# Optimization experiments

Hardware: AMD Instinct MI355X
Metric: run time of the kernel (lower is better)

The kernel has to match this reference:

```python
import jax, jax.numpy as jnp
import numpy as np

B, N = 32, 1000
HID, COM = 256, 64
T_LEN, NOP = 288, 3
NVAL, TP_D, CS_D, TIME_D = 9, 2, 4, 4
IN_C = CS_D + TP_D + NVAL            # 15, competition GAT input
IN_CO = IN_C + COM                    # 79, cooperation GAT input
OBS = TIME_D + TP_D + CS_D + 2 * COM + NVAL  # 147
K_D = K_F = 500                       # int(0.5*N + 0.5)
TEMP = 1.0
NEG = jnp.float32(-1e8)


def setup_inputs() -> dict:
    key = jax.random.key(0)
    ks = jax.random.split(key, 24)
    def nrm(k, shp, scale=0.05):
        return (jax.random.normal(k, shp, dtype=jnp.float32) * scale)
    return {
        "time_idx": jax.random.randint(ks[0], (B, N), 0, T_LEN, dtype=jnp.int32),
        "op_idx": jax.random.randint(ks[1], (B, N), 0, NOP, dtype=jnp.int32),
        "value_feats": jax.random.normal(ks[2], (B, N, NVAL), dtype=jnp.float32),
        "dpcs_mark": jax.random.randint(ks[3], (B, N, 1), 0, 2) > 0,
        "adj_comp": jax.random.randint(ks[4], (B, N, N), 0, 2) > 0,
        "adj_coop": jax.random.randint(ks[5], (B, N, N), 0, 2) > 0,
        "distance": jax.random.uniform(ks[6], (N, N), dtype=jnp.float32),
        "time_tab": jax.random.uniform(ks[7], (T_LEN, TIME_D), dtype=jnp.float32),
        "tp_tab": jax.random.uniform(ks[8], (NOP, TP_D), dtype=jnp.float32),
        "cs_tab": jax.random.uniform(ks[9], (N, CS_D), dtype=jnp.float32),
        "Wc": nrm(ks[10], (IN_C, COM)),
        "asrc_c": nrm(ks[11], (COM,)),
        "adst_c": nrm(ks[12], (COM,)),
        "wd_c": jnp.float32(0.1),
        "Wco": nrm(ks[13], (IN_CO, COM)),
        "asrc_co": nrm(ks[14], (COM,)),
        "adst_co": nrm(ks[15], (COM,)),
        "wd_co": jnp.float32(0.1),
        "Wp": nrm(ks[16], (OBS, HID)),
        "bp": jnp.zeros((HID,), dtype=jnp.float32),
        "vpd": nrm(ks[17], (HID,)),
        "vpf": nrm(ks[18], (HID,)),
    }


def gat(x, W, a_src, a_dst, w_d, adj, dist):
    """Single-head GAT over dense boolean adjacency. adj[b,j,i] True => edge j->i."""
    h = jnp.einsum("bnf,fd->bnd", x, W)                       # (B,N,D)
    e = (jnp.einsum("bid,d->bi", h, a_dst)[:, :, None]        # dst term
         + jnp.einsum("bjd,d->bj", h, a_src)[:, None, :]      # src term
         + w_d * dist.T[None])                                 # dist[j,i] edge feat
    e = jax.nn.leaky_relu(e, 0.2)
    mask = jnp.swapaxes(adj, 1, 2)                             # (B, dst i, src j)
    e = jnp.where(mask, e, NEG)
    alpha = jax.nn.softmax(e, axis=-1)
    alpha = jnp.where(mask, alpha, 0.0)                        # isolated nodes -> 0
    return jax.nn.elu(jnp.einsum("bij,bjd->bid", alpha, h))


def gated_pool(x_p, scores, valid, k, temp):
    scores = scores - scores.max(axis=1, keepdims=True)
    scores = jnp.where(valid, scores, NEG)                     # (B,N,1)
    val_topk = jax.lax.top_k(scores[..., 0], k)[0]             # (B,k)
    min_topk = val_topk.min(axis=-1)[:, None, None]
    scores = jnp.where(scores < min_topk, NEG, scores)
    w = jax.nn.softmax(scores / temp, axis=1)
    xg = x_p * w
    return jnp.concatenate([xg.sum(axis=1), xg.max(axis=1)], axis=-1)  # (B,2H)


def reference(time_idx, op_idx, value_feats, dpcs_mark, adj_comp, adj_coop,
              distance, time_tab, tp_tab, cs_tab, Wc, asrc_c, adst_c, wd_c,
              Wco, asrc_co, adst_co, wd_co, Wp, bp, vpd, vpf):
    time_e = time_tab[time_idx]                                # (B,N,4)
    tp_e = tp_tab[op_idx]                                      # (B,N,2)
    cs_e = jnp.broadcast_to(cs_tab[None], (B, N, CS_D))        # (B,N,4)
    vf_det = jax.lax.stop_gradient(value_feats)
    x = jnp.concatenate([cs_e, tp_e, vf_det], axis=-1)         # (B,N,15)
    comp_reps = gat(x, Wc, asrc_c, adst_c, wd_c, adj_comp, distance)
    x_m = jnp.concatenate([x, comp_reps], axis=-1)             # (B,N,79)
    coop_reps = gat(x_m, Wco, asrc_co, adst_co, wd_co, adj_coop, distance)
    sag = jnp.concatenate([time_e, cs_e, tp_e, value_feats, comp_reps, coop_reps], axis=-1)
    x_p = jnp.einsum("bnf,fh->bnh", sag, Wp) + bp              # (B,N,HID)
    scores_d = jnp.einsum("bnh,h->bn", x_p, vpd)[..., None]
    s_d = gated_pool(x_p, scores_d, dpcs_mark, K_D, TEMP)
    scores_f = jnp.einsum("bnh,h->bn", x_p, vpf)[..., None]
    s_f = gated_pool(x_p, scores_f, ~dpcs_mark, K_F, TEMP)
    return jnp.concatenate([s_f, s_d], axis=-1)                # (B, 4*HID)
```

## Files before the change

### kernel.cpp

```cpp
#include <hip/hip_runtime.h>
#include <hip/hip_bf16.h>

#define NB 32
#define NN 1000
#define COMD 64
#define HIDD 256
#define KSEL 500
#define TI 16
#define GATX ((NN + TI - 1) / TI)
#define PACKX 32
#define NSPL 32
#define ROWS 32
#define DSTRIDE 1024

#define PB_AQ1  0
#define PB_DT   1024
#define PB_WP   1280
#define PB_WCO  1320
#define PB_MISC 1344
#define PB_EMB  1345
#define PB_N    (PB_EMB + NB * NN / 4)

typedef __hip_bfloat16 bf16;
typedef unsigned long long u64;
typedef __attribute__((ext_vector_type(4))) float f32x4;
typedef __attribute__((ext_vector_type(8))) short s16x8;
typedef __attribute__((ext_vector_type(4))) short s16x4;
typedef __attribute__((ext_vector_type(4))) unsigned short u16x4;
typedef __attribute__((ext_vector_type(2))) unsigned long long u64x2;

__device__ __forceinline__ float b2f(bf16 x){ return __bfloat162float(x); }

template<bool F32>
__device__ __forceinline__ float ldf(const void* p, long i){
  return F32 ? ((const float*)p)[i] : b2f(((const bf16*)p)[i]);
}
__device__ __forceinline__ float ldr(const void* p, long i, int f32){
  return f32 ? ((const float*)p)[i] : b2f(((const bf16*)p)[i]);
}
template<bool BINT>
__device__ __forceinline__ bool ldb(const void* p, long i){
  return BINT ? (((const int*)p)[i] != 0) : (((const unsigned char*)p)[i] != 0);
}

__device__ __forceinline__ float wave_sum(float v){
#pragma unroll
  for (int o = 32; o > 0; o >>= 1) v += __shfl_down(v, o, 64);
  return v;
}
__device__ __forceinline__ float wave_bsum(float v){
#pragma unroll
  for (int o = 32; o > 0; o >>= 1) v += __shfl_xor(v, o, 64);
  return v;
}
__device__ __forceinline__ float wave_bmax(float v){
#pragma unroll
  for (int o = 32; o > 0; o >>= 1) v = fmaxf(v, __shfl_xor(v, o, 64));
  return v;
}
__device__ __forceinline__ int wave_bsum_i(int v){
#pragma unroll
  for (int o = 32; o > 0; o >>= 1) v += __shfl_xor(v, o, 64);
  return v;
}
__device__ __forceinline__ unsigned fkey(float f){
  unsigned u = __float_as_uint(f);
  return (u & 0x80000000u) ? ~u : (u | 0x80000000u);
}
__device__ __forceinline__ void split_bf(float v, short& hi, short& lo){
  unsigned u = __float_as_uint(v);
  float hf = __uint_as_float(u & 0xFFFF0000u);
  hi = (short)(u >> 16);
  float r = v - hf;
  lo = (short)(__float_as_uint(r) >> 16);
}
__device__ __forceinline__ short f2bs(float v){
  bf16 h = __float2bfloat16(v);
  short s; __builtin_memcpy(&s, &h, 2); return s;
}
__device__ __forceinline__ void hB_write(short* hB_hi, short* hB_lo,
                                         int b, int n, int ch, float v){
  int kb = n >> 5, g4 = (n >> 3) & 3, u = n & 7;
  long off = ((((long)b * 32 + kb) * 4 + g4) * 64 + ch) * 8 + u;
  short hi, lo; split_bf(v, hi, lo);
  hB_hi[off] = hi; hB_lo[off] = lo;
}
__device__ __forceinline__ void sniff2(const void* dist, const void* adjc,
                                       int lane, int& f32, int& as_int){
  unsigned wdist = ((const unsigned*)dist)[lane];
  unsigned wadj  = ((const unsigned*)adjc)[lane];
  f32 = (__ballot((wdist & 0xFFFFu) >= 0x8000u) != 0ull) ? 1 : 0;
  as_int = (__ballot(wadj > 1u) == 0ull) ? 1 : 0;
}

#define SMEM_BYTES 8704

template<bool F32>
__device__ __forceinline__ void dist_t_role(const void* dist, bf16* distTb,
                                            int rel, void* sm){
  bf16 (*tile)[68] = (bf16 (*)[68])sm;
  int t = threadIdx.x;
  int wv = t >> 6, lane = t & 63;
  int it = (rel & 15) * 64, jt = (rel >> 4) * 64;
#pragma unroll
  for (int r = 0; r < 16; ++r){
    int jl = r * 4 + wv;
    int j = jt + jl, i = it + lane;
    float v = (j < NN && i < NN) ? ldf<F32>(dist, (long)j * NN + i) : 0.f;
    tile[jl][lane] = __float2bfloat16(v);
  }
  __syncthreads();
#pragma unroll
  for (int r = 0; r < 16; ++r){
    int il = r * 4 + wv;
    int i = it + il, j = jt + lane;
    if (i < NN) distTb[(long)i * DSTRIDE + j] = tile[lane][il];
  }
}
template<bool BINT>
__device__ __forceinline__ void adjq_role(const void* adj, u64* adjQ,
                                          int rel, void* sm){
  u64 (*aw)[33] = (u64 (*)[33])sm;
  int t = threadIdx.x;
  int wv = t >> 6, lane = t & 63;
  int j0 = (rel & 31) * 32;
  int b  = rel >> 5;
  int ch3 = (192 + lane < 250) ? (192 + lane) : 249;
  int chk[4] = { lane, 64 + lane, 128 + lane, ch3 };
  long row0;
  {
    int j = j0 + wv * 8;
    int jc = (j < NN) ? j : (NN - 1);
    row0 = ((long)b * NN + jc) * (long)NN;
  }
  if (BINT){
    const int* base = (const int*)adj;
    uint4 cur[4], nxt[4];
#pragma unroll
    for (int c = 0; c < 4; ++c)
      cur[c] = *(const uint4*)(base + row0 + (long)chk[c] * 4);
#pragma unroll
    for (int r = 0; r < 8; ++r){
      if (r < 7){
        int j2 = j0 + wv * 8 + r + 1;
        int jc2 = (j2 < NN) ? j2 : (NN - 1);
        long row2 = ((long)b * NN + jc2) * (long)NN;
#pragma unroll
        for (int c = 0; c < 4; ++c)
          nxt[c] = *(const uint4*)(base + row2 + (long)chk[c] * 4);
      }
      int j = j0 + wv * 8 + r;
#pragma unroll
      for (int c = 0; c < 4; ++c){
        u64 bal0 = __ballot(cur[c].x != 0u);
        u64 bal1 = __ballot(cur[c].y != 0u);
        u64 bal2 = __ballot(cur[c].z != 0u);
        u64 bal3 = __ballot(cur[c].w != 0u);
        if (lane < 4){
          u64 w = 0;
          if (j < NN){
            int sh = 16 * lane;
            w = ((bal0 >> sh) & 0xFFFFull)
              | (((bal1 >> sh) & 0xFFFFull) << 16)
              | (((bal2 >> sh) & 0xFFFFull) << 32)
              | (((bal3 >> sh) & 0xFFFFull) << 48);
          }
          aw[c * 4 + lane][wv * 8 + r] = w;
        }
      }
      if (r < 7){
#pragma unroll
        for (int c = 0; c < 4; ++c) cur[c] = nxt[c];
      }
    }
  } else {
    const unsigned char* base = (const unsigned char*)adj;
    unsigned cur[4], nxt[4];
#pragma unroll
    for (int c = 0; c < 4; ++c)
      cur[c] = *(const unsigned*)(base + row0 + (long)chk[c] * 4);
#pragma unroll
    for (int r = 0; r < 8; ++r){
      if (r < 7){
        int j2 = j0 + wv * 8 + r + 1;
        int jc2 = (j2 < NN) ? j2 : (NN - 1);
        long row2 = ((long)b * NN + jc2) * (long)NN;
#pragma unroll
        for (int c = 0; c < 4; ++c)
          nxt[c] = *(const unsigned*)(base + row2 + (long)chk[c] * 4);
      }
      int j = j0 + wv * 8 + r;
#pragma unroll
      for (int c = 0; c < 4; ++c){
        u64 bal0 = __ballot((cur[c] & 0xFFu) != 0u);
        u64 bal1 = __ballot((cur[c] & 0xFF00u) != 0u);
        u64 bal2 = __ballot((cur[c] & 0xFF0000u) != 0u);
        u64 bal3 = __ballot((cur[c] & 0xFF000000u) != 0u);
        if (lane < 4){
          u64 w = 0;
          if (j < NN){
            int sh = 16 * lane;
            w = ((bal0 >> sh) & 0xFFFFull)
              | (((bal1 >> sh) & 0xFFFFull) << 16)
              | (((bal2 >> sh) & 0xFFFFull) << 32)
              | (((bal3 >> sh) & 0xFFFFull) << 48);
          }
          aw[c * 4 + lane][wv * 8 + r] = w;
        }
      }
      if (r < 7){
#pragma unroll
        for (int c = 0; c < 4; ++c) cur[c] = nxt[c];
      }
    }
  }
  __syncthreads();
#pragma unroll
  for (int rr = 0; rr < 2; ++rr){
    int w2 = t + rr * 256;
    int iw = w2 >> 5, jloc = w2 & 31;
    adjQ[((long)b * 16 + iw) * 1024 + j0 + jloc] = aw[iw][jloc];
  }
}
template<bool F32>
__device__ __forceinline__ void wp_role(const void* Wp, const void* vpd, const void* vpf,
                        short* WpB_hi, short* WpB_lo, float* wv_ws, int rel){
  int t = threadIdx.x;
  int g = t >> 6, lane = t & 63;
  int f = rel * 4 + g;
  float wrow[4];
#pragma unroll
  for (int r = 0; r < 4; ++r){
    int ch = r * 64 + lane;
    wrow[r] = (f < 147) ? ldf<F32>(Wp, (long)f * HIDD + ch) : 0.f;
  }
  int kb = f >> 5, q = (f >> 3) & 3, u = f & 7;
#pragma unroll
  for (int r = 0; r < 4; ++r){
    int ch = r * 64 + lane;
    long off = (((long)(kb * 4 + q)) * 256 + ch) * 8 + u;
    short hi, lo; split_bf(wrow[r], hi, lo);
    WpB_hi[off] = hi; WpB_lo[off] = lo;
  }
  float ad = 0.f, af = 0.f;
#pragma unroll
  for (int r = 0; r < 4; ++r){
    int ch = r * 64 + lane;
    ad += wrow[r] * ldf<F32>(vpd, ch);
    af += wrow[r] * ldf<F32>(vpf, ch);
  }
  ad = wave_bsum(ad); af = wave_bsum(af);
  if (lane == 0){ wv_ws[f] = ad; wv_ws[160 + f] = af; }
}
template<bool F32>
__device__ __forceinline__ void wco_role(const void* Wco, const void* asrc, const void* adst,
                         short* WcoB_hi, short* WcoB_lo, float* pvco, int rel){
  int t = threadIdx.x;
  int g = t >> 6, lane = t & 63;
  int f = rel * 4 + g;
  float w = (f < 79) ? ldf<F32>(Wco, (long)f * COMD + lane) : 0.f;
  int kb = f >> 5, q = (f >> 3) & 3, u = f & 7;
  long off = (((long)(kb * 4 + q)) * 64 + lane) * 8 + u;
  short hi, lo; split_bf(w, hi, lo);
  WcoB_hi[off] = hi; WcoB_lo[off] = lo;
  float dd = wave_bsum(w * ldf<F32>(adst, lane));
  float ss = wave_bsum(w * ldf<F32>(asrc, lane));
  if (lane == 0){ pvco[f] = dd; pvco[96 + f] = ss; }
}
template<bool F32>
__device__ __forceinline__ void misc_role(const void* wdc, const void* wdco,
                          const void* bp, const void* vpd, const void* vpf,
                          int f32, int as_int,
                          int* flags, float* wd_ws, float* wv_ws){
  int t = threadIdx.x;
  if (t >= 64) return;
  int lane = t;
  float ad = 0.f, af = 0.f;
#pragma unroll
  for (int r = 0; r < 4; ++r){
    int ch = r * 64 + lane;
    float bb = ldf<F32>(bp, ch);
    ad += bb * ldf<F32>(vpd, ch);
    af += bb * ldf<F32>(vpf, ch);
  }
  ad = wave_bsum(ad); af = wave_bsum(af);
  if (lane == 0){
    wv_ws[320] = ad; wv_ws[321] = af;
    wd_ws[0] = ldf<F32>(wdc, 0);
    wd_ws[1] = ldf<F32>(wdco, 0);
    flags[0] = f32; flags[1] = as_int;
  }
}
template<bool F32>
__device__ __forceinline__ void embed_body(
    const int* op_idx, const void* vf, const void* cs_tab, const void* tp_tab,
    const void* Wc, const void* asrc, const void* adst,
    float* x_out, short* hB_hi, short* hB_lo, float* ed_out, float* es_out,
    int rel){
  int t = threadIdx.x;
  int w = t >> 6, lane = t & 63;
  int g = rel * 4 + w;
  int b = g / NN, n = g - b * NN;
  int op = op_idx[g];
  float xv = 0.f, hacc = 0.f;
#pragma unroll
  for (int f = 0; f < 15; ++f){
    float x_f;
    if (f < 4)      x_f = ldf<F32>(cs_tab, n * 4 + f);
    else if (f < 6) x_f = ldf<F32>(tp_tab, op * 2 + (f - 4));
    else            x_f = ldf<F32>(vf, (long)g * 9 + (f - 6));
    if (lane == f) xv = x_f;
    hacc += x_f * ldf<F32>(Wc, f * COMD + lane);
  }
  if (lane < 15) x_out[g * 15 + lane] = xv;
  hB_write(hB_hi, hB_lo, b, n, lane, hacc);
  float sd = wave_sum(hacc * ldf<F32>(adst, lane));
  float ss = wave_sum(hacc * ldf<F32>(asrc, lane));
  if (lane == 0){ ed_out[g] = sd; es_out[g] = ss; }
}
__global__ void __launch_bounds__(256) k_prep(
    const void* dist, const void* adj_comp,
    const void* wdc, const void* wdco,
    const void* Wp, const void* vpd, const void* vpf, const void* bp,
    const void* Wco, const void* asrc_co, const void* adst_co,
    const int* op_idx, const void* vfeat, const void* cs_tab, const void* tp_tab,
    const void* Wc, const void* asrc_c, const void* adst_c,
    int* flags, float* wd_ws, bf16* distTb, u64* adjQc,
    short* WpB_hi, short* WpB_lo, float* wv_ws,
    short* WcoB_hi, short* WcoB_lo, float* pvco,
    float* x_ws, short* hB_hi, short* hB_lo, float* ed_c, float* es_c){
  __shared__ __attribute__((aligned(16))) char smem[SMEM_BYTES];
  int blk = blockIdx.x;
  int f32, as_int;
  sniff2(dist, adj_comp, threadIdx.x & 63, f32, as_int);
  if (blk < PB_DT){
    if (as_int) adjq_role<true >(adj_comp, adjQc, blk - PB_AQ1, smem);
    else        adjq_role<false>(adj_comp, adjQc, blk - PB_AQ1, smem);
  } else if (blk < PB_WP){
    if (f32) dist_t_role<true >(dist, distTb, blk - PB_DT, smem);
    else     dist_t_role<false>(dist, distTb, blk - PB_DT, smem);
  } else if (blk < PB_WCO){
    if (f32) wp_role<true >(Wp, vpd, vpf, WpB_hi, WpB_lo, wv_ws, blk - PB_WP);
    else     wp_role<false>(Wp, vpd, vpf, WpB_hi, WpB_lo, wv_ws, blk - PB_WP);
  } else if (blk < PB_MISC){
    if (f32) wco_role<true >(Wco, asrc_co, adst_co, WcoB_hi, WcoB_lo, pvco, blk - PB_WCO);
    else     wco_role<false>(Wco, asrc_co, adst_co, WcoB_hi, WcoB_lo, pvco, blk - PB_WCO);
  } else if (blk < PB_EMB){
    if (f32) misc_role<true >(wdc, wdco, bp, vpd, vpf, f32, as_int, flags, wd_ws, wv_ws);
    else     misc_role<false>(wdc, wdco, bp, vpd, vpf, f32, as_int, flags, wd_ws, wv_ws);
  } else {
    if (f32) embed_body<true >(op_idx, vfeat, cs_tab, tp_tab, Wc, asrc_c, adst_c,
                               x_ws, hB_hi, hB_lo, ed_c, es_c, blk - PB_EMB);
    else     embed_body<false>(op_idx, vfeat, cs_tab, tp_tab, Wc, asrc_c, adst_c,
                               x_ws, hB_hi, hB_lo, ed_c, es_c, blk - PB_EMB);
  }
}

template<int MODE>
__device__ __forceinline__ void gat_body(
    const float* __restrict__ ed, const float* __restrict__ es,
    const float* __restrict__ wd_ws, int wd_idx, const u64* __restrict__ adjQ,
    const bf16* __restrict__ distTb,
    const short* __restrict__ hB_hi, const short* __restrict__ hB_lo,
    float* __restrict__ reps,
    const int* __restrict__ flags, const void* adj_raw, u64* adjQ_out,
    const float* __restrict__ x_ws,
    const short* __restrict__ WcoB_hi, const short* __restrict__ WcoB_lo,
    const float* __restrict__ pvco,
    short* hB2_hi, short* hB2_lo, float* ed_o, float* es_o,
    const int* __restrict__ time_idx, const int* __restrict__ op_idx,
    const void* vf, const void* time_tab, const void* cs_tab, const void* tp_tab,
    const float* __restrict__ comp,
    const short* __restrict__ WpB_hi, const short* __restrict__ WpB_lo,
    const float* __restrict__ wv_ws, const void* bp,
    float* x_p, float* scf_o, float* scd_o){
  __shared__ short pA[32 * 544] __attribute__((aligned(16)));
  __shared__ float redz[TI][4];
  __shared__ float esred[4];
  if (MODE == 0 && blockIdx.x >= GATX){
    int rel = (blockIdx.x - GATX) * NB + blockIdx.y;
    if (flags[1]) adjq_role<true >(adj_raw, adjQ_out, rel, (void*)pA);
    else          adjq_role<false>(adj_raw, adjQ_out, rel, (void*)pA);
    return;
  }
  int t = threadIdx.x;
  int wv = t >> 6, lane = t & 63;
  int b = blockIdx.y;
  int i0 = blockIdx.x * TI;
  float wd = wd_ws[wd_idx];
  int iw = i0 >> 6;
  int sb2 = (i0 & 63) >> 2;
  int j0 = t * 4;

  const u64* aq = adjQ + ((long)b * 16 + iw) * 1024 + j0;
  u64x2 wA = *(const u64x2*)&aq[0];
  u64x2 wB = *(const u64x2*)&aq[2];
  u64 wsh[4] = { wA[0] >> sb2, wA[1] >> sb2, wB[0] >> sb2, wB[1] >> sb2 };
  float4 es4 = *(const float4*)&es[(long)b * NN + j0];
  float esv[4] = {es4.x, es4.y, es4.z, es4.w};
  float esm = -1e30f;
#pragma unroll
  for (int c = 0; c < 4; ++c)
    esm = fmaxf(esm, (j0 + c < NN) ? esv[c] : -1e30f);
  esm = wave_bmax(esm);
  if (lane == 0) esred[wv] = esm;

  float ed_i[TI]; float edm = -1e30f;
#pragma unroll
  for (int ti = 0; ti < TI; ++ti){
    int i = i0 + ti;
    float ev = ed[(long)b * NN + ((i < NN) ? i : (NN - 1))];
    ed_i[ti] = ev;
    edm = fmaxf(edm, (i < NN) ? ev : -1e30f);
  }
  __syncthreads();
  float M = fmaxf(fmaxf(esred[0], esred[1]), fmaxf(esred[2], esred[3]))
            + edm + fmaxf(wd, 0.f);
  M = fmaxf(M, 0.f);

  float p[TI][4];
  const bf16* dbase = distTb + j0;
#pragma unroll
  for (int ti = 0; ti < TI; ++ti){
    int i = i0 + ti;
    int ic = (i < NN) ? i : (NN - 1);
    u16x4 d4 = *(const u16x4*)&dbase[(long)ic * DSTRIDE];
    float edti = ed_i[ti];
    int psh = 16 * (ti & 3) + (ti >> 2);
#pragma unroll
    for (int c = 0; c < 4; ++c){
      float d = __uint_as_float((unsigned)d4[c] << 16);
      float v = edti + esv[c] + wd * d;
      v = fmaxf(v, 0.2f * v);
      bool edge = (wsh[c] >> psh) & 1ull;
      float e = edge ? v : -1e30f;
      p[ti][c] = __expf(e - M);
    }
  }

  int kbw = 8 * wv + (lane >> 3);
  int qw = (lane >> 1) & 3;
  int u0 = 4 * (lane & 1);
  int wbase = kbw * 544 + qw * 136 + u0;
#pragma unroll
  for (int ti = 0; ti < TI; ++ti){
    float zs = p[ti][0] + p[ti][1] + p[ti][2] + p[ti][3];
    zs = wave_bsum(zs);
    if (lane == 0) redz[ti][wv] = zs;
    s16x4 s4 = { f2bs(p[ti][0]), f2bs(p[ti][1]), f2bs(p[ti][2]), f2bs(p[ti][3]) };
    *(s16x4*)&pA[wbase + ti * 8] = s4;
  }
  __syncthreads();

  int q = lane >> 4, m = lane & 15;
  int abase = q * 136 + m * 8;
  int ch = wv * 16 + m;
  const short* bh = hB_hi + (long)b * 65536 + ((long)q * 64 + ch) * 8;
  const short* bl = hB_lo + (long)b * 65536 + ((long)q * 64 + ch) * 8;
  f32x4 acc = {0.f, 0.f, 0.f, 0.f};
#pragma unroll
  for (int kb = 0; kb < 32; ++kb){
    s16x8 a   = *(const s16x8*)&pA[kb * 544 + abase];
    s16x8 bhi = *(const s16x8*)&bh[(long)kb * 2048];
    s16x8 blo = *(const s16x8*)&bl[(long)kb * 2048];
    acc = __builtin_amdgcn_mfma_f32_16x16x32_bf16(a, bhi, acc, 0, 0, 0);
    acc = __builtin_amdgcn_mfma_f32_16x16x32_bf16(a, blo, acc, 0, 0, 0);
  }
  float vr[4];
#pragma unroll
  for (int reg = 0; reg < 4; ++reg){
    int ti = (lane >> 4) * 4 + reg;
    float z = redz[ti][0] + redz[ti][1] + redz[ti][2] + redz[ti][3];
    float zi = (z > 0.f) ? 1.f / z : 0.f;
    float v = acc[reg] * zi;
    v = (v > 0.f) ? v : expm1f(v);
    vr[reg] = v;
    if (MODE == 0){
      int ch2 = wv * 16 + (lane & 15);
      if (i0 + ti < NN)
        reps[((long)b * NN + i0 + ti) * COMD + ch2] = v;
    }
  }

  if (MODE == 0){
    __syncthreads();
    float* cx = (float*)pA;
    short* cA_hi = pA + 2560;
    short* cA_lo = pA + 2560 + 1920;
    {
      int ch2 = wv * 16 + (lane & 15);
#pragma unroll
      for (int reg = 0; reg < 4; ++reg){
        int row = (lane >> 4) * 4 + reg;
        cx[row * 80 + 15 + ch2] = vr[reg];
      }
    }
    for (int idx = t; idx < 16 * 15; idx += 256){
      int nl = idx / 15, f = idx - nl * 15;
      int i = i0 + nl; int ic = (i < NN) ? i : (NN - 1);
      cx[nl * 80 + f] = x_ws[((long)b * NN + ic) * 15 + f];
    }
    __syncthreads();
    {
      int node = t >> 4, sub = t & 15;
      float dd = 0.f, ss = 0.f;
      for (int f = sub; f < 79; f += 16){
        float c = cx[node * 80 + f];
        dd += c * pvco[f];
        ss += c * pvco[96 + f];
      }
#pragma unroll
      for (int o = 8; o > 0; o >>= 1){
        dd += __shfl_xor(dd, o, 64);
        ss += __shfl_xor(ss, o, 64);
      }
      if (sub == 0 && i0 + node < NN){
        ed_o[(long)b * NN + i0 + node] = dd;
        es_o[(long)b * NN + i0 + node] = ss;
      }
    }
    for (int idx = t; idx < 16 * 96; idx += 256){
      int mm = idx / 96, k = idx - mm * 96;
      float v = (k < 79) ? cx[mm * 80 + k] : 0.f;
      int kb = k >> 5, qq = (k >> 3) & 3, u = k & 7;
      short hi, lo; split_bf(v, hi, lo);
      int off = (kb * 16 + mm) * 40 + qq * 8 + u;
      cA_hi[off] = hi; cA_lo[off] = lo;
    }
    __syncthreads();
    {
      int q2 = lane >> 4, m2 = lane & 15;
      int ch3 = wv * 16 + m2;
      f32x4 a2 = {0.f, 0.f, 0.f, 0.f};
#pragma unroll
      for (int kb = 0; kb < 3; ++kb){
        int aoff = (kb * 16 + m2) * 40 + q2 * 8;
        s16x8 a_hi = *(const s16x8*)&cA_hi[aoff];
        s16x8 a_lo = *(const s16x8*)&cA_lo[aoff];
        long boff = (((long)(kb * 4 + q2)) * 64 + ch3) * 8;
        s16x8 b_hi = *(const s16x8*)&WcoB_hi[boff];
        s16x8 b_lo = *(const s16x8*)&WcoB_lo[boff];
        a2 = __builtin_amdgcn_mfma_f32_16x16x32_bf16(a_hi, b_hi, a2, 0, 0, 0);
        a2 = __builtin_amdgcn_mfma_f32_16x16x32_bf16(a_hi, b_lo, a2, 0, 0, 0);
        a2 = __builtin_amdgcn_mfma_f32_16x16x32_bf16(a_lo, b_hi, a2, 0, 0, 0);
      }
#pragma unroll
      for (int reg = 0; reg < 4; ++reg){
        int row = (lane >> 4) * 4 + reg;
        int n2 = i0 + row;
        hB_write(hB2_hi, hB2_lo, b, n2, ch3, a2[reg]);
      }
    }
  } else {
    __syncthreads();
    float* sagF = (float*)pA;
    short* sgA_hi = pA + 4736;
    short* sgA_lo = pA + 7936;
    int f32 = flags[0];
    {
      int ch2 = wv * 16 + (lane & 15);
#pragma unroll
      for (int reg = 0; reg < 4; ++reg){
        int row = (lane >> 4) * 4 + reg;
        sagF[row * 148 + 83 + ch2] = vr[reg];
      }
    }
    for (int idx = t; idx < 16 * 83; idx += 256){
      int nl = idx / 83, f = idx - nl * 83;
      int n = i0 + nl; int ic = (n < NN) ? n : (NN - 1);
      long g = (long)b * NN + ic;
      float v;
      if (f < 4)       v = ldr(time_tab, (long)time_idx[g] * 4 + f, f32);
      else if (f < 8)  v = ldr(cs_tab, ic * 4 + (f - 4), f32);
      else if (f < 10) v = ldr(tp_tab, (long)op_idx[g] * 2 + (f - 8), f32);
      else if (f < 19) v = ldr(vf, g * 9 + (f - 10), f32);
      else             v = comp[g * COMD + (f - 19)];
      sagF[nl * 148 + f] = v;
    }
    __syncthreads();
    for (int idx = t; idx < 16 * 160; idx += 256){
      int mm = idx / 160, k = idx - mm * 160;
      float v = (k < 147) ? sagF[mm * 148 + k] : 0.f;
      int kb = k >> 5, qq = (k >> 3) & 3, u = k & 7;
      short hi, lo; split_bf(v, hi, lo);
      int off = (kb * 16 + mm) * 40 + qq * 8 + u;
      sgA_hi[off] = hi; sgA_lo[off] = lo;
    }
    {
      int node = t >> 4, sub = t & 15;
      float ad = 0.f, af = 0.f;
      for (int f = sub; f < 147; f += 16){
        float s = sagF[node * 148 + f];
        ad += s * wv_ws[f];
        af += s * wv_ws[160 + f];
      }
#pragma unroll
      for (int o = 8; o > 0; o >>= 1){
        ad += __shfl_xor(ad, o, 64);
        af += __shfl_xor(af, o, 64);
      }
      if (sub == 0 && i0 + node < NN){
        scd_o[(long)b * NN + i0 + node] = ad + wv_ws[320];
        scf_o[(long)b * NN + i0 + node] = af + wv_ws[321];
      }
    }
    __syncthreads();
    int Ag = lane >> 4, Am = lane & 15;
    f32x4 acc2[4] = {{0,0,0,0},{0,0,0,0},{0,0,0,0},{0,0,0,0}};
#pragma unroll
    for (int kb = 0; kb < 5; ++kb){
      int aoff = (kb * 16 + Am) * 40 + Ag * 8;
      s16x8 a_hi = *(const s16x8*)&sgA_hi[aoff];
      s16x8 a_lo = *(const s16x8*)&sgA_lo[aoff];
#pragma unroll
      for (int ct = 0; ct < 4; ++ct){
        int ch3 = wv * 64 + ct * 16 + Am;
        long boff = (((long)(kb * 4 + Ag)) * 256 + ch3) * 8;
        s16x8 b_hi = *(const s16x8*)&WpB_hi[boff];
        s16x8 b_lo = *(const s16x8*)&WpB_lo[boff];
        acc2[ct] = __builtin_amdgcn_mfma_f32_16x16x32_bf16(a_hi, b_hi, acc2[ct], 0, 0, 0);
        acc2[ct] = __builtin_amdgcn_mfma_f32_16x16x32_bf16(a_hi, b_lo, acc2[ct], 0, 0, 0);
        acc2[ct] = __builtin_amdgcn_mfma_f32_16x16x32_bf16(a_lo, b_hi, acc2[ct], 0, 0, 0);
      }
    }
#pragma unroll
    for (int ct = 0; ct < 4; ++ct){
      int ch3 = wv * 64 + ct * 16 + (lane & 15);
      float bb = ldr(bp, ch3, f32);
#pragma unroll
      for (int reg = 0; reg < 4; ++reg){
        int row = (lane >> 4) * 4 + reg;
        if (i0 + row < NN)
          x_p[((long)b * NN + i0 + row) * HIDD + ch3] = acc2[ct][reg] + bb;
      }
    }
  }
}
__global__ void __launch_bounds__(256) k_gat1(
    const float* ed, const float* es, const float* wd_ws, const u64* adjQ,
    const bf16* distTb, const short* hB_hi, const short* hB_lo, float* reps,
    const int* flags, const void* adj_raw, u64* adjQ_out,
    const float* x_ws, const short* WcoB_hi, const short* WcoB_lo,
    const float* pvco, short* hB2_hi, short* hB2_lo, float* ed_o, float* es_o){
  gat_body<0>(ed, es, wd_ws, 0, adjQ, distTb, hB_hi, hB_lo, reps,
              flags, adj_raw, adjQ_out, x_ws, WcoB_hi, WcoB_lo, pvco,
              hB2_hi, hB2_lo, ed_o, es_o,
              nullptr, nullptr, nullptr, nullptr, nullptr, nullptr,
              nullptr, nullptr, nullptr, nullptr, nullptr,
              nullptr, nullptr, nullptr);
}
__global__ void __launch_bounds__(256) k_gat2x(
    const float* ed, const float* es, const float* wd_ws, const u64* adjQ,
    const bf16* distTb, const short* hB_hi, const short* hB_lo,
    const int* flags,
    const int* time_idx, const int* op_idx, const void* vf,
    const void* time_tab, const void* cs_tab, const void* tp_tab,
    const float* comp, const short* WpB_hi, const short* WpB_lo,
    const float* wv_ws, const void* bp,
    float* x_p, float* scf, float* scd){
  gat_body<1>(ed, es, wd_ws, 1, adjQ, distTb, hB_hi, hB_lo, nullptr,
              flags, nullptr, nullptr, nullptr, nullptr, nullptr, nullptr,
              nullptr, nullptr, nullptr, nullptr,
              time_idx, op_idx, vf, time_tab, cs_tab, tp_tab,
              comp, WpB_hi, WpB_lo, wv_ws, bp, x_p, scf, scd);
}

template<bool BINT>
__device__ __forceinline__ void topk_body(
    const float* scf, const float* scd, const void* mark, float* wls){
  int lane = threadIdx.x;
  int b = blockIdx.x, pool = blockIdx.y;
  const float* sc = (pool == 0) ? scf : scd;
  float v[16]; unsigned key[16];
  float m0 = -INFINITY;
#pragma unroll
  for (int r = 0; r < 16; ++r){
    int n = r * 64 + lane;
    float s = (n < NN) ? sc[b * NN + n] : -INFINITY;
    v[r] = s;
    m0 = fmaxf(m0, s);
  }
  m0 = wave_bmax(m0);
  float m1 = -INFINITY;
#pragma unroll
  for (int r = 0; r < 16; ++r){
    int n = r * 64 + lane;
    bool valid = false;
    if (n < NN){
      bool mk = ldb<BINT>(mark, b * NN + n);
      valid = (pool == 0) ? !mk : mk;
    }
    v[r] = valid ? (v[r] - m0) : -1e8f;
    key[r] = fkey(v[r]);
    if (n < NN) m1 = fmaxf(m1, v[r]);
  }
  m1 = wave_bmax(m1);

  unsigned lo = 0u, hi = 0xFFFFFFFFu;
  while (lo < hi){
    unsigned mid = lo + ((hi - lo) >> 1) + 1u;
    int c = 0;
#pragma unroll
    for (int r = 0; r < 16; ++r) c += (key[r] >= mid) ? 1 : 0;
    c = wave_bsum_i(c);
    if (c >= KSEL) lo = mid; else hi = mid - 1u;
  }

  float p[16];
  float ls = 0.f;
#pragma unroll
  for (int r = 0; r < 16; ++r){
    int n = r * 64 + lane;
    float pp = (n < NN && key[r] >= lo) ? __expf(v[r] - m1) : 0.f;
    p[r] = pp;
    ls += pp;
  }
  ls = wave_bsum(ls);
  float zinv = (ls > 0.f) ? 1.f / ls : 0.f;
  float* w_out = wls + ((long)b * 2 + pool) * 1024;
#pragma unroll
  for (int r = 0; r < 16; ++r){
    int n = r * 64 + lane;
    if (n < NN) w_out[n] = p[r] * zinv;
  }
}
__global__ void k_topk(const int* flags, const float* scf, const float* scd,
                       const void* mark, float* wls){
  if (flags[1]) topk_body<true >(scf, scd, mark, wls);
  else          topk_body<false>(scf, scd, mark, wls);
}

__global__ void __launch_bounds__(256) k_psum(
    const float* __restrict__ wls, const float* __restrict__ x_p,
    float* __restrict__ part){
  __shared__ float wf[ROWS], wdd[ROWS];
  int t = threadIdx.x;
  int b = blockIdx.x, z = blockIdx.y;
  int n0 = z * ROWS;
  int ns = min(ROWS, NN - n0);
  if (t < ns){
    wf[t]  = wls[((long)b * 2 + 0) * 1024 + n0 + t];
    wdd[t] = wls[((long)b * 2 + 1) * 1024 + n0 + t];
  }
  __syncthreads();
  float sf = 0.f, mf = -INFINITY, sd = 0.f, md = -INFINITY;
  const float* xb = x_p + ((long)b * NN + n0) * HIDD + t;
  for (int k = 0; k < ns; ++k){
    float xv = xb[(long)k * HIDD];
    float gf = wf[k] * xv;
    float gd = wdd[k] * xv;
    sf += gf; mf = fmaxf(mf, gf);
    sd += gd; md = fmaxf(md, gd);
  }
  long pb = (((long)b * NSPL + z) * 4) * HIDD + t;
  part[pb + 0 * HIDD] = sf;
  part[pb + 1 * HIDD] = mf;
  part[pb + 2 * HIDD] = sd;
  part[pb + 3 * HIDD] = md;
}

template<bool F32>
__device__ __forceinline__ void pfin_body(const float* part, void* out){
  int t = threadIdx.x;
  int b = blockIdx.x;
  float sf = 0.f, mf = -INFINITY, sd = 0.f, md = -INFINITY;
#pragma unroll
  for (int z = 0; z < NSPL; ++z){
    long pb = (((long)b * NSPL + z) * 4) * HIDD + t;
    sf += part[pb + 0 * HIDD];
    mf = fmaxf(mf, part[pb + 1 * HIDD]);
    sd += part[pb + 2 * HIDD];
    md = fmaxf(md, part[pb + 3 * HIDD]);
  }
  long ob = (long)b * 1024;
  if (F32){
    ((float*)out)[ob + t] = sf;
    ((float*)out)[ob + 256 + t] = mf;
    ((float*)out)[ob + 512 + t] = sd;
    ((float*)out)[ob + 768 + t] = md;
  } else {
    ((bf16*)out)[ob + t] = __float2bfloat16(sf);
    ((bf16*)out)[ob + 256 + t] = __float2bfloat16(mf);
    ((bf16*)out)[ob + 512 + t] = __float2bfloat16(sd);
    ((bf16*)out)[ob + 768 + t] = __float2bfloat16(md);
  }
}
__global__ void k_pfin(const int* flags, const float* part, void* out){
  if (flags[0]) pfin_body<true >(part, out);
  else          pfin_body<false>(part, out);
}

extern "C" void kernel_launch(void* const* d_in, const int* in_sizes, int n_in,
                              void* d_out, int out_size, void* d_ws, size_t ws_size,
                              hipStream_t stream){
  const int*  time_idx = (const int*)d_in[0];
  const int*  op_idx   = (const int*)d_in[1];
  const void* vfeat    = d_in[2];
  const void* dpcs     = d_in[3];
  const void* adj_comp = d_in[4];
  const void* adj_coop = d_in[5];
  const void* dist     = d_in[6];
  const void* time_tab = d_in[7];
  const void* tp_tab   = d_in[8];
  const void* cs_tab   = d_in[9];
  const void* Wc       = d_in[10];
  const void* asrc_c   = d_in[11];
  const void* adst_c   = d_in[12];
  const void* wd_c     = d_in[13];
  const void* Wco      = d_in[14];
  const void* asrc_co  = d_in[15];
  const void* adst_co  = d_in[16];
  const void* wd_co    = d_in[17];
  const void* Wp       = d_in[18];
  const void* bp       = d_in[19];
  const void* vpd      = d_in[20];
  const void* vpf      = d_in[21];

  char* ws = (char*)d_ws;
  size_t o = 0;
  auto alloc = [&](size_t bytes)->char*{
    char* p = ws + o; o = (o + bytes + 255) & ~(size_t)255; return p;
  };
  int*   flags   = (int*)alloc(16);
  float* wd_ws   = (float*)alloc(8);
  bf16*  distTb  = (bf16*)alloc((size_t)NN * DSTRIDE * 2);
  u64*   adjQc   = (u64*)alloc((size_t)NB * 16 * 1024 * 8);
  u64*   adjQo   = (u64*)alloc((size_t)NB * 16 * 1024 * 8);
  float* x_ws    = (float*)alloc((size_t)NB * NN * 15 * 4);
  float* comp    = (float*)alloc((size_t)NB * NN * COMD * 4);
  short* hB_hi   = (short*)alloc((size_t)NB * 65536 * 2);
  short* hB_lo   = (short*)alloc((size_t)NB * 65536 * 2);
  short* hB2_hi  = (short*)alloc((size_t)NB * 65536 * 2);
  short* hB2_lo  = (short*)alloc((size_t)NB * 65536 * 2);
  short* WpB_hi  = (short*)alloc((size_t)5 * 4 * 256 * 8 * 2);
  short* WpB_lo  = (short*)alloc((size_t)5 * 4 * 256 * 8 * 2);
  short* WcoB_hi = (short*)alloc((size_t)3 * 4 * 64 * 8 * 2);
  short* WcoB_lo = (short*)alloc((size_t)3 * 4 * 64 * 8 * 2);
  float* wv_ws   = (float*)alloc(322 * 4);
  float* pvco    = (float*)alloc(192 * 4);
  float* ed_c    = (float*)alloc((size_t)NB * NN * 4 + 256);
  float* es_c    = (float*)alloc((size_t)NB * NN * 4 + 256);
  float* ed_o    = (float*)alloc((size_t)NB * NN * 4 + 256);
  float* es_o    = (float*)alloc((size_t)NB * NN * 4 + 256);
  float* scf     = (float*)alloc((size_t)NB * NN * 4);
  float* scd     = (float*)alloc((size_t)NB * NN * 4);
  float* wls     = (float*)alloc((size_t)NB * 2 * 1024 * 4);
  float* part    = (float*)alloc((size_t)NB * NSPL * 4 * HIDD * 4);
  float* x_p     = (float*)alloc((size_t)NB * NN * HIDD * 4);

  k_prep<<<dim3(PB_N), dim3(256), 0, stream>>>(
      dist, adj_comp, wd_c, wd_co, Wp, vpd, vpf, bp,
      Wco, asrc_co, adst_co,
      op_idx, vfeat, cs_tab, tp_tab, Wc, asrc_c, adst_c,
      flags, wd_ws, distTb, adjQc, WpB_hi, WpB_lo, wv_ws,
      WcoB_hi, WcoB_lo, pvco,
      x_ws, hB_hi, hB_lo, ed_c, es_c);
  k_gat1<<<dim3(GATX + PACKX, NB), dim3(256), 0, stream>>>(
      ed_c, es_c, wd_ws, adjQc, distTb, hB_hi, hB_lo, comp,
      flags, adj_coop, adjQo,
      x_ws, WcoB_hi, WcoB_lo, pvco, hB2_hi, hB2_lo, ed_o, es_o);
  k_gat2x<<<dim3(GATX, NB), dim3(256), 0, stream>>>(
      ed_o, es_o, wd_ws, adjQo, distTb, hB2_hi, hB2_lo,
      flags, time_idx, op_idx, vfeat, time_tab, cs_tab, tp_tab,
      comp, WpB_hi, WpB_lo, wv_ws, bp, x_p, scf, scd);
  k_topk<<<dim3(NB, 2), dim3(64), 0, stream>>>(flags, scf, scd, dpcs, wls);
  k_psum<<<dim3(NB, NSPL), dim3(256), 0, stream>>>(wls, x_p, part);
  k_pfin<<<dim3(NB), dim3(256), 0, stream>>>(flags, part, d_out);
}
```

Baseline: 453.7 us.

## Read raw adjacency directly in GAT kernels instead of prepacking bitmasks

```diff
diff --git a/kernel.cpp b/kernel.cpp
--- a/kernel.cpp
+++ b/kernel.cpp
@@ -8,17 +8,15 @@
 #define KSEL 500
 #define TI 16
 #define GATX ((NN + TI - 1) / TI)
-#define PACKX 32
 #define NSPL 32
 #define ROWS 32
 #define DSTRIDE 1024
 
-#define PB_AQ1  0
-#define PB_DT   1024
-#define PB_WP   1280
-#define PB_WCO  1320
-#define PB_MISC 1344
-#define PB_EMB  1345
+#define PB_DT   0
+#define PB_WP   256
+#define PB_WCO  296
+#define PB_MISC 320
+#define PB_EMB  321
 #define PB_N    (PB_EMB + NB * NN / 4)
 
 typedef __hip_bfloat16 bf16;
@@ -27,7 +25,6 @@
 typedef __attribute__((ext_vector_type(8))) short s16x8;
 typedef __attribute__((ext_vector_type(4))) short s16x4;
 typedef __attribute__((ext_vector_type(4))) unsigned short u16x4;
-typedef __attribute__((ext_vector_type(2))) unsigned long long u64x2;
 
 __device__ __forceinline__ float b2f(bf16 x){ return __bfloat162float(x); }
 
@@ -115,111 +112,6 @@
     int il = r * 4 + wv;
     int i = it + il, j = jt + lane;
     if (i < NN) distTb[(long)i * DSTRIDE + j] = tile[lane][il];
-  }
-}
-template<bool BINT>
-__device__ __forceinline__ void adjq_role(const void* adj, u64* adjQ,
-                                          int rel, void* sm){
-  u64 (*aw)[33] = (u64 (*)[33])sm;
-  int t = threadIdx.x;
-  int wv = t >> 6, lane = t & 63;
-  int j0 = (rel & 31) * 32;
-  int b  = rel >> 5;
-  int ch3 = (192 + lane < 250) ? (192 + lane) : 249;
-  int chk[4] = { lane, 64 + lane, 128 + lane, ch3 };
-  long row0;
-  {
-    int j = j0 + wv * 8;
-    int jc = (j < NN) ? j : (NN - 1);
-    row0 = ((long)b * NN + jc) * (long)NN;
-  }
-  if (BINT){
-    const int* base = (const int*)adj;
-    uint4 cur[4], nxt[4];
-#pragma unroll
-    for (int c = 0; c < 4; ++c)
-      cur[c] = *(const uint4*)(base + row0 + (long)chk[c] * 4);
-#pragma unroll
-    for (int r = 0; r < 8; ++r){
-      if (r < 7){
-        int j2 = j0 + wv * 8 + r + 1;
-        int jc2 = (j2 < NN) ? j2 : (NN - 1);
-        long row2 = ((long)b * NN + jc2) * (long)NN;
-#pragma unroll
-        for (int c = 0; c < 4; ++c)
-          nxt[c] = *(const uint4*)(base + row2 + (long)chk[c] * 4);
-      }
-      int j = j0 + wv * 8 + r;
-#pragma unroll
-      for (int c = 0; c < 4; ++c){
-        u64 bal0 = __ballot(cur[c].x != 0u);
-        u64 bal1 = __ballot(cur[c].y != 0u);
-        u64 bal2 = __ballot(cur[c].z != 0u);
-        u64 bal3 = __ballot(cur[c].w != 0u);
-        if (lane < 4){
-          u64 w = 0;
-          if (j < NN){
-            int sh = 16 * lane;
-            w = ((bal0 >> sh) & 0xFFFFull)
-              | (((bal1 >> sh) & 0xFFFFull) << 16)
-              | (((bal2 >> sh) & 0xFFFFull) << 32)
-              | (((bal3 >> sh) & 0xFFFFull) << 48);
-          }
-          aw[c * 4 + lane][wv * 8 + r] = w;
-        }
-      }
-      if (r < 7){
-#pragma unroll
-        for (int c = 0; c < 4; ++c) cur[c] = nxt[c];
-      }
-    }
-  } else {
-    const unsigned char* base = (const unsigned char*)adj;
-    unsigned cur[4], nxt[4];
-#pragma unroll
-    for (int c = 0; c < 4; ++c)
-      cur[c] = *(const unsigned*)(base + row0 + (long)chk[c] * 4);
-#pragma unroll
-    for (int r = 0; r < 8; ++r){
-      if (r < 7){
-        int j2 = j0 + wv * 8 + r + 1;
-        int jc2 = (j2 < NN) ? j2 : (NN - 1);
-        long row2 = ((long)b * NN + jc2) * (long)NN;
-#pragma unroll
-        for (int c = 0; c < 4; ++c)
-          nxt[c] = *(const unsigned*)(base + row2 + (long)chk[c] * 4);
-      }
-      int j = j0 + wv * 8 + r;
-#pragma unroll
-      for (int c = 0; c < 4; ++c){
-        u64 bal0 = __ballot((cur[c] & 0xFFu) != 0u);
-        u64 bal1 = __ballot((cur[c] & 0xFF00u) != 0u);
-        u64 bal2 = __ballot((cur[c] & 0xFF0000u) != 0u);
-        u64 bal3 = __ballot((cur[c] & 0xFF000000u) != 0u);
-        if (lane < 4){
-          u64 w = 0;
-          if (j < NN){
-            int sh = 16 * lane;
-            w = ((bal0 >> sh) & 0xFFFFull)
-              | (((bal1 >> sh) & 0xFFFFull) << 16)
-              | (((bal2 >> sh) & 0xFFFFull) << 32)
-              | (((bal3 >> sh) & 0xFFFFull) << 48);
-          }
-          aw[c * 4 + lane][wv * 8 + r] = w;
-        }
-      }
-      if (r < 7){
-#pragma unroll
-        for (int c = 0; c < 4; ++c) cur[c] = nxt[c];
-      }
-    }
-  }
-  __syncthreads();
-#pragma unroll
-  for (int rr = 0; rr < 2; ++rr){
-    int w2 = t + rr * 256;
-    int iw = w2 >> 5, jloc = w2 & 31;
-    adjQ[((long)b * 16 + iw) * 1024 + j0 + jloc] = aw[iw][jloc];
   }
 }
 template<bool F32>
@@ -325,7 +217,7 @@
     const void* Wco, const void* asrc_co, const void* adst_co,
     const int* op_idx, const void* vfeat, const void* cs_tab, const void* tp_tab,
     const void* Wc, const void* asrc_c, const void* adst_c,
-    int* flags, float* wd_ws, bf16* distTb, u64* adjQc,
+    int* flags, float* wd_ws, bf16* distTb,
     short* WpB_hi, short* WpB_lo, float* wv_ws,
     short* WcoB_hi, short* WcoB_lo, float* pvco,
     float* x_ws, short* hB_hi, short* hB_lo, float* ed_c, float* es_c){
@@ -333,10 +225,7 @@
   int blk = blockIdx.x;
   int f32, as_int;
   sniff2(dist, adj_comp, threadIdx.x & 63, f32, as_int);
-  if (blk < PB_DT){
-    if (as_int) adjq_role<true >(adj_comp, adjQc, blk - PB_AQ1, smem);
-    else        adjq_role<false>(adj_comp, adjQc, blk - PB_AQ1, smem);
-  } else if (blk < PB_WP){
+  if (blk < PB_WP){
     if (f32) dist_t_role<true >(dist, distTb, blk - PB_DT, smem);
     else     dist_t_role<false>(dist, distTb, blk - PB_DT, smem);
   } else if (blk < PB_WCO){
@@ -359,11 +248,11 @@
 template<int MODE>
 __device__ __forceinline__ void gat_body(
     const float* __restrict__ ed, const float* __restrict__ es,
-    const float* __restrict__ wd_ws, int wd_idx, const u64* __restrict__ adjQ,
+    const float* __restrict__ wd_ws, int wd_idx,
     const bf16* __restrict__ distTb,
     const short* __restrict__ hB_hi, const short* __restrict__ hB_lo,
     float* __restrict__ reps,
-    const int* __restrict__ flags, const void* adj_raw, u64* adjQ_out,
+    const int* __restrict__ flags, const void* __restrict__ adj_raw,
     const float* __restrict__ x_ws,
     const short* __restrict__ WcoB_hi, const short* __restrict__ WcoB_lo,
     const float* __restrict__ pvco,
@@ -377,25 +266,61 @@
   __shared__ short pA[32 * 544] __attribute__((aligned(16)));
   __shared__ float redz[TI][4];
   __shared__ float esred[4];
-  if (MODE == 0 && blockIdx.x >= GATX){
-    int rel = (blockIdx.x - GATX) * NB + blockIdx.y;
-    if (flags[1]) adjq_role<true >(adj_raw, adjQ_out, rel, (void*)pA);
-    else          adjq_role<false>(adj_raw, adjQ_out, rel, (void*)pA);
-    return;
-  }
   int t = threadIdx.x;
   int wv = t >> 6, lane = t & 63;
   int b = blockIdx.y;
   int i0 = blockIdx.x * TI;
   float wd = wd_ws[wd_idx];
-  int iw = i0 >> 6;
-  int sb2 = (i0 & 63) >> 2;
   int j0 = t * 4;
 
-  const u64* aq = adjQ + ((long)b * 16 + iw) * 1024 + j0;
-  u64x2 wA = *(const u64x2*)&aq[0];
-  u64x2 wB = *(const u64x2*)&aq[2];
-  u64 wsh[4] = { wA[0] >> sb2, wA[1] >> sb2, wB[0] >> sb2, wB[1] >> sb2 };
+  unsigned am[4];
+  int ib = (i0 + 16 <= NN) ? i0 : (NN - 16);
+  int sh = i0 - ib;
+  {
+    int bint = flags[1];
+    if (bint){
+      const int* abase = (const int*)adj_raw + ((long)b * NN) * NN + ib;
+#pragma unroll
+      for (int c = 0; c < 4; ++c){
+        int j = j0 + c;
+        unsigned m = 0u;
+        if (j < NN){
+          const int* rp = abase + (long)j * NN;
+          uint4 d0 = *(const uint4*)(rp + 0);
+          uint4 d1 = *(const uint4*)(rp + 4);
+          uint4 d2 = *(const uint4*)(rp + 8);
+          uint4 d3 = *(const uint4*)(rp + 12);
+          m = (unsigned)(d0.x != 0)        | ((unsigned)(d0.y != 0) << 1)
+            | ((unsigned)(d0.z != 0) << 2) | ((unsigned)(d0.w != 0) << 3)
+            | ((unsigned)(d1.x != 0) << 4) | ((unsigned)(d1.y != 0) << 5)
+            | ((unsigned)(d1.z != 0) << 6) | ((unsigned)(d1.w != 0) << 7)
+            | ((unsigned)(d2.x != 0) << 8) | ((unsigned)(d2.y != 0) << 9)
+            | ((unsigned)(d2.z != 0) << 10)| ((unsigned)(d2.w != 0) << 11)
+            | ((unsigned)(d3.x != 0) << 12)| ((unsigned)(d3.y != 0) << 13)
+            | ((unsigned)(d3.z != 0) << 14)| ((unsigned)(d3.w != 0) << 15);
+        }
+        am[c] = m;
+      }
+    } else {
+      const unsigned char* abase = (const unsigned char*)adj_raw + (long)b * NN * NN + ib;
+#pragma unroll
+      for (int c = 0; c < 4; ++c){
+        int j = j0 + c;
+        unsigned m = 0u;
+        if (j < NN){
+          const u64* rp = (const u64*)(abase + (long)j * NN);
+          u64 w0 = rp[0], w1 = rp[1];
+#pragma unroll
+          for (int k = 0; k < 8; ++k){
+            m |= (unsigned)(((w0 >> (8 * k)) & 0xFFull) != 0) << k;
+            m |= (unsigned)(((w1 >> (8 * k)) & 0xFFull) != 0) << (k + 8);
+          }
+        }
+        am[c] = m;
+      }
+    }
+  }
+
   float4 es4 = *(const float4*)&es[(long)b * NN + j0];
   float esv[4] = {es4.x, es4.y, es4.z, es4.w};
   float esm = -1e30f;
@@ -426,13 +351,13 @@
     int ic = (i < NN) ? i : (NN - 1);
     u16x4 d4 = *(const u16x4*)&dbase[(long)ic * DSTRIDE];
     float edti = ed_i[ti];
-    int psh = 16 * (ti & 3) + (ti >> 2);
+    int kbit = ti + sh;
 #pragma unroll
     for (int c = 0; c < 4; ++c){
       float d = __uint_as_float((unsigned)d4[c] << 16);
       float v = edti + esv[c] + wd * d;
       v = fmaxf(v, 0.2f * v);
-      bool edge = (wsh[c] >> psh) & 1ull;
+      bool edge = (am[c] >> kbit) & 1u;
       float e = edge ? v : -1e30f;
       p[ti][c] = __expf(e - M);
     }
@@ -637,29 +562,29 @@
   }
 }
 __global__ void __launch_bounds__(256) k_gat1(
-    const float* ed, const float* es, const float* wd_ws, const u64* adjQ,
+    const float* ed, const float* es, const float* wd_ws,
     const bf16* distTb, const short* hB_hi, const short* hB_lo, float* reps,
-    const int* flags, const void* adj_raw, u64* adjQ_out,
+    const int* flags, const void* adj_raw,
     const float* x_ws, const short* WcoB_hi, const short* WcoB_lo,
     const float* pvco, short* hB2_hi, short* hB2_lo, float* ed_o, float* es_o){
-  gat_body<0>(ed, es, wd_ws, 0, adjQ, distTb, hB_hi, hB_lo, reps,
-              flags, adj_raw, adjQ_out, x_ws, WcoB_hi, WcoB_lo, pvco,
+  gat_body<0>(ed, es, wd_ws, 0, distTb, hB_hi, hB_lo, reps,
+              flags, adj_raw, x_ws, WcoB_hi, WcoB_lo, pvco,
               hB2_hi, hB2_lo, ed_o, es_o,
               nullptr, nullptr, nullptr, nullptr, nullptr, nullptr,
               nullptr, nullptr, nullptr, nullptr, nullptr,
               nullptr, nullptr, nullptr);
 }
 __global__ void __launch_bounds__(256) k_gat2x(
-    const float* ed, const float* es, const float* wd_ws, const u64* adjQ,
+    const float* ed, const float* es, const float* wd_ws,
     const bf16* distTb, const short* hB_hi, const short* hB_lo,
-    const int* flags,
+    const int* flags, const void* adj_raw,
     const int* time_idx, const int* op_idx, const void* vf,
     const void* time_tab, const void* cs_tab, const void* tp_tab,
     const float* comp, const short* WpB_hi, const short* WpB_lo,
     const float* wv_ws, const void* bp,
     float* x_p, float* scf, float* scd){
-  gat_body<1>(ed, es, wd_ws, 1, adjQ, distTb, hB_hi, hB_lo, nullptr,
-              flags, nullptr, nullptr, nullptr, nullptr, nullptr, nullptr,
+  gat_body<1>(ed, es, wd_ws, 1, distTb, hB_hi, hB_lo, nullptr,
+              flags, adj_raw, nullptr, nullptr, nullptr, nullptr,
               nullptr, nullptr, nullptr, nullptr,
               time_idx, op_idx, vf, time_tab, cs_tab, tp_tab,
               comp, WpB_hi, WpB_lo, wv_ws, bp, x_p, scf, scd);
@@ -824,8 +749,6 @@
   int*   flags   = (int*)alloc(16);
   float* wd_ws   = (float*)alloc(8);
   bf16*  distTb  = (bf16*)alloc((size_t)NN * DSTRIDE * 2);
-  u64*   adjQc   = (u64*)alloc((size_t)NB * 16 * 1024 * 8);
-  u64*   adjQo   = (u64*)alloc((size_t)NB * 16 * 1024 * 8);
   float* x_ws    = (float*)alloc((size_t)NB * NN * 15 * 4);
   float* comp    = (float*)alloc((size_t)NB * NN * COMD * 4);
   short* hB_hi   = (short*)alloc((size_t)NB * 65536 * 2);
@@ -852,16 +775,17 @@
       dist, adj_comp, wd_c, wd_co, Wp, vpd, vpf, bp,
       Wco, asrc_co, adst_co,
       op_idx, vfeat, cs_tab, tp_tab, Wc, asrc_c, adst_c,
-      flags, wd_ws, distTb, adjQc, WpB_hi, WpB_lo, wv_ws,
+      flags, wd_ws, distTb, WpB_hi, WpB_lo, wv_ws,
       WcoB_hi, WcoB_lo, pvco,
       x_ws, hB_hi, hB_lo, ed_c, es_c);
-  k_gat1<<<dim3(GATX + PACKX, NB), dim3(256), 0, stream>>>(
-      ed_c, es_c, wd_ws, adjQc, distTb, hB_hi, hB_lo, comp,
-      flags, adj_coop, adjQo,
+  k_gat1<<<dim3(GATX, NB), dim3(256), 0, stream>>>(
+      ed_c, es_c, wd_ws, distTb, hB_hi, hB_lo, comp,
+      flags, adj_comp,
       x_ws, WcoB_hi, WcoB_lo, pvco, hB2_hi, hB2_lo, ed_o, es_o);
   k_gat2x<<<dim3(GATX, NB), dim3(256), 0, stream>>>(
-      ed_o, es_o, wd_ws, adjQo, distTb, hB2_hi, hB2_lo,
-      flags, time_idx, op_idx, vfeat, time_tab, cs_tab, tp_tab,
+      ed_o, es_o, wd_ws, distTb, hB2_hi, hB2_lo,
+      flags, adj_coop,
+      time_idx, op_idx, vfeat, time_tab, cs_tab, tp_tab,
       comp, WpB_hi, WpB_lo, wv_ws, bp, x_p, scf, scd);
   k_topk<<<dim3(NB, 2), dim3(64), 0, stream>>>(flags, scf, scd, dpcs, wls);
   k_psum<<<dim3(NB, NSPL), dim3(256), 0, stream>>>(wls, x_p, part);
```

After: 475.8 us. 4.9% more time.
